# Kernel tuning notes

Measured on AMD Instinct MI355X. Metric: run time of the kernel, lower is better.

Reference implementation:

```python
import jax, jax.numpy as jnp
import numpy as np
from jax import lax

B, N, C = 4, 16384, 256
NH, HD = 8, 32          # num_heads, head_dim
SR = 4                  # spatial reduction ratio
LMAX = 6144             # max per-batch query length (static pad size)
QLENS = np.array([2048, 6144, 3072, 5120], dtype=np.int32)
TQ = int(QLENS.sum())   # 16384 total ragged queries
SCALE = HD ** -0.5


def setup_inputs() -> dict:
    key = jax.random.key(0)
    ks = jax.random.split(key, 6)
    w = lambda k, s: jax.random.normal(k, s, jnp.float32) * 0.02
    return {
        "x": jax.random.normal(ks[0], (B, N, C), jnp.float32),
        "q": jax.random.normal(ks[1], (TQ, C), jnp.float32),
        "H": 128,
        "W": 128,
        "q_lengths": jnp.asarray(QLENS),
        "w_q": w(ks[2], (C, C)),        # stored [in, out] (= torch W.T)
        "w_kv": w(ks[3], (C, 2 * C)),
        "sr_w": w(ks[4], (C, C, SR, SR)),  # OIHW
        "sr_b": jnp.zeros((C,), jnp.float32),
        "ln_g": jnp.ones((C,), jnp.float32),
        "ln_b": jnp.zeros((C,), jnp.float32),
        "proj_w": w(ks[5], (C, C)),
        "proj_b": jnp.zeros((C,), jnp.float32),
    }


def reference(x, q, H, W, q_lengths, w_q, w_kv, sr_w, sr_b, ln_g, ln_b, proj_w, proj_b):
    # q projection -> per-head ragged queries [NH, TQ, HD]
    qh = (q @ w_q).reshape(TQ, NH, HD).transpose(1, 0, 2)

    # spatial reduction of KV source: conv(k=SR, stride=SR) + LayerNorm
    x_ = x.transpose(0, 2, 1).reshape(B, C, H, W)
    x_ = lax.conv_general_dilated(x_, sr_w, (SR, SR), "VALID",
                                  dimension_numbers=("NCHW", "OIHW", "NCHW"))
    x_ = x_ + sr_b[None, :, None, None]
    x_ = x_.reshape(B, C, -1).transpose(0, 2, 1)  # [B, Nkv, C]
    mu = x_.mean(-1, keepdims=True)
    var = ((x_ - mu) ** 2).mean(-1, keepdims=True)
    x_ = (x_ - mu) * lax.rsqrt(var + 1e-5) * ln_g + ln_b

    # kv projection -> [NH, B, Nkv, HD] each
    kv = (x_ @ w_kv).reshape(B, -1, 2, NH, HD)
    k = kv[:, :, 0].transpose(2, 0, 1, 3)
    v = kv[:, :, 1].transpose(2, 0, 1, 3)

    # ragged -> padded layout for the variable-length attention
    batch_ids = jnp.repeat(jnp.arange(B), q_lengths, total_repeat_length=TQ)
    offsets = jnp.cumsum(q_lengths) - q_lengths
    pos = jnp.arange(TQ) - offsets[batch_ids]
    qp = jnp.zeros((NH, B, LMAX, HD), qh.dtype).at[:, batch_ids, pos].set(qh)

    # per-batch attention over reduced keys (padded rows are discarded below)
    attn = jax.nn.softmax(jnp.einsum("hbld,hbkd->hblk", qp, k) * SCALE, axis=-1)
    op = jnp.einsum("hblk,hbkd->hbld", attn, v)

    # gather valid ragged outputs back: [NH, TQ, HD] -> [TQ, C]
    o = op[:, batch_ids, pos].transpose(1, 0, 2).reshape(TQ, C)
    return o @ proj_w + proj_b
```

## Files before the change

### kernel.cpp

```cpp
#include <hip/hip_runtime.h>
#include <hip/hip_bf16.h>


using bf16 = __hip_bfloat16;
using f32x4 = __attribute__((ext_vector_type(4))) float;
using bf16x8 = __attribute__((ext_vector_type(8))) short;

#define DEVINL __device__ __forceinline__
#define AS1 __attribute__((address_space(1)))
#define AS3 __attribute__((address_space(3)))

DEVINL f32x4 mfma16(bf16x8 a, bf16x8 b, f32x4 c) {
    return __builtin_amdgcn_mfma_f32_16x16x32_bf16(a, b, c, 0, 0, 0);
}

DEVINL unsigned short f2bf(float f) {
    union { float f; unsigned u; } x; x.f = f;
    unsigned u = x.u;
    u += 0x7fffu + ((u >> 16) & 1u);
    return (unsigned short)(u >> 16);
}

DEVINL unsigned pk_rtz(float a, float b) {
    return __builtin_amdgcn_perm(__float_as_uint(b), __float_as_uint(a), 0x07060302u);
}

DEVINL float ex2(float x) { return __builtin_amdgcn_exp2f(x); }

DEVINL void gl16(const bf16* g, bf16* l) {
    __builtin_amdgcn_global_load_lds(
        (const AS1 void*)(unsigned long long)(uintptr_t)g,
        (AS3 void*)(unsigned)(uintptr_t)l, 16, 0, 0);
}
DEVINL void gl16f(const float* g, float* l) {
    __builtin_amdgcn_global_load_lds(
        (const AS1 void*)(unsigned long long)(uintptr_t)g,
        (AS3 void*)(unsigned)(uintptr_t)l, 16, 0, 0);
}

__global__ __launch_bounds__(256) void prep_kernel(
    const float* __restrict__ w_q, const float* __restrict__ w_kv,
    const float* __restrict__ proj_w, const float* __restrict__ sr_w,
    const float* __restrict__ q,
    bf16* __restrict__ wqT, bf16* __restrict__ wkvT, bf16* __restrict__ wprT,
    bf16* __restrict__ wcv, bf16* __restrict__ q_bf)
{
    const int bb = blockIdx.x;
    if (bb < 256) {
        int idx = bb * 256 + threadIdx.x;
        int k = idx & 255, n = idx >> 8;
        wqT[idx] = __float2bfloat16(w_q[k * 256 + n]);
    } else if (bb < 768) {
        int idx = (bb - 256) * 256 + threadIdx.x;
        int k = idx & 255, n = idx >> 8;
        wkvT[idx] = __float2bfloat16(w_kv[k * 512 + n]);
    } else if (bb < 1024) {
        int idx = (bb - 768) * 256 + threadIdx.x;
        int k = idx & 255, n = idx >> 8;
        wprT[idx] = __float2bfloat16(proj_w[k * 256 + n]);
    } else if (bb < 5120) {
        int idx = (bb - 1024) * 256 + threadIdx.x;
        int o = idx >> 12, rest = idx & 4095, dydx = rest >> 8, c = rest & 255;
        wcv[idx] = __float2bfloat16(sr_w[((o << 8) + c) * 16 + dydx]);
    } else {
        int i = (bb - 5120) * 256 + threadIdx.x;
        float4 a = ((const float4*)q)[i * 2];
        float4 b = ((const float4*)q)[i * 2 + 1];
        uint4 u;
        u.x = f2bf(a.x) | ((unsigned)f2bf(a.y) << 16);
        u.y = f2bf(a.z) | ((unsigned)f2bf(a.w) << 16);
        u.z = f2bf(b.x) | ((unsigned)f2bf(b.y) << 16);
        u.w = f2bf(b.z) | ((unsigned)f2bf(b.w) << 16);
        ((uint4*)q_bf)[i] = u;
    }
}

template<int EMODE>
__global__ __launch_bounds__(256, 4) void gemm_kernel(
    const bf16* __restrict__ A, const bf16* __restrict__ WT,
    const float* __restrict__ bias,
    bf16* __restrict__ outb, float* __restrict__ outf, bf16* __restrict__ out2,
    int M, int N, int K, int KS)
{
    __shared__ alignas(16) bf16 As[2][64 * 64];
    __shared__ alignas(16) bf16 Bs[2][64 * 64];
    const int cpx = gridDim.x >> 3;
    const int bx = (blockIdx.x & 7) * cpx + (blockIdx.x >> 3);
    const int ntn = N >> 6;
    const int tm = bx / ntn, tn = bx % ntn;
    const int tid = threadIdx.x, lane = tid & 63, wid = tid >> 6;
    const int l15 = lane & 15, g = lane >> 4;
    const int wm = (wid >> 1) << 5, wn = (wid & 1) << 5;
    f32x4 acc[2][2] = {};

    int r_[2], cs_[2];
#pragma unroll
    for (int j = 0; j < 2; ++j) {
        int idx = (wid * 2 + j) * 64 + lane;
        r_[j] = idx >> 3;
        cs_[j] = ((idx & 7) ^ (r_[j] & 7)) << 3;
    }
    const bf16* Arow = &A[(size_t)(tm * 64) * K];
    const bf16* Brow = &WT[(size_t)(tn * 64) * K];

    const int kbeg = blockIdx.y * KS;
    const int nsteps = KS >> 6;

    auto stage = [&](int buf, int k0) {
#pragma unroll
        for (int j = 0; j < 2; ++j) {
            gl16(Arow + (size_t)r_[j] * K + (k0 + cs_[j]), &As[buf][(wid * 2 + j) * 512]);
            gl16(Brow + (size_t)r_[j] * K + (k0 + cs_[j]), &Bs[buf][(wid * 2 + j) * 512]);
        }
    };

    stage(0, kbeg);
    __syncthreads();

    for (int t = 0; t < nsteps; ++t) {
        const int buf = t & 1;
        if (t + 1 < nsteps) stage(buf ^ 1, kbeg + (t + 1) * 64);
#pragma unroll
        for (int kk = 0; kk < 2; ++kk) {
            const int sw = l15 & 7;
            const int co = ((kk * 4 + g) ^ sw) << 3;
            bf16x8 a0 = *(const bf16x8*)&As[buf][(wm + l15) * 64 + co];
            bf16x8 a1 = *(const bf16x8*)&As[buf][(wm + 16 + l15) * 64 + co];
            bf16x8 b0 = *(const bf16x8*)&Bs[buf][(wn + l15) * 64 + co];
            bf16x8 b1 = *(const bf16x8*)&Bs[buf][(wn + 16 + l15) * 64 + co];
            acc[0][0] = mfma16(a0, b0, acc[0][0]);
            acc[0][1] = mfma16(a0, b1, acc[0][1]);
            acc[1][0] = mfma16(a1, b0, acc[1][0]);
            acc[1][1] = mfma16(a1, b1, acc[1][1]);
        }
        __syncthreads();
    }

    const float qscale = 0.1767766953f * 1.4426950409f;
#pragma unroll
    for (int mi = 0; mi < 2; ++mi)
#pragma unroll
    for (int ni = 0; ni < 2; ++ni)
#pragma unroll
    for (int r = 0; r < 4; ++r) {
        int row = tm * 64 + wm + mi * 16 + g * 4 + r;
        int col = tn * 64 + wn + ni * 16 + l15;
        float v = acc[mi][ni][r];
        if constexpr (EMODE == 0) {
            outb[(size_t)row * 256 + col] = __float2bfloat16(v * qscale);
        } else if constexpr (EMODE == 1) {
            outf[(size_t)row * 256 + col] = v + bias[col];
        } else if constexpr (EMODE == 2) {
            int bb = row >> 10, key = row & 1023;
            if (col < 256) {
                int hh = col >> 5, d = col & 31;
                outb[(size_t)(((bb << 3) + hh) * 1024 + key) * 32 + d] = __float2bfloat16(v);
            } else {
                int d = col - 256;
                int c = key & 31;
                int pos = (((c >> 2) & 3) << 3) + ((c >> 4) << 2) + (c & 3);
                int keyp = (key & ~31) | pos;
                out2[(size_t)(((bb << 3) + (d >> 5)) * 32 + (d & 31)) * 1024 + keyp] =
                    __float2bfloat16(v);
            }
        }
    }
}

__global__ __launch_bounds__(256, 6) void conv_gemm_kernel(
    const float* __restrict__ X, const bf16* __restrict__ WT,
    float* __restrict__ partials)
{
    __shared__ alignas(16) float Af[2][64 * 32];
    __shared__ alignas(16) bf16 Bs[2][64 * 32];
    const int K = 4096;
    const int swz = (blockIdx.x & 7) * 256 + (blockIdx.x >> 3);
    const int combo = swz >> 6;
    const int tm = swz & 63;
    const int tn = combo >> 3, slice = combo & 7;
    const int tid = threadIdx.x, lane = tid & 63, wid = tid >> 6;
    const int l15 = lane & 15, g = lane >> 4;
    const int wm = (wid >> 1) << 5, wn = (wid & 1) << 5;
    f32x4 acc[2][2] = {};

    size_t laneoffA[2];
#pragma unroll
    for (int j = 0; j < 2; ++j) {
        int call = wid * 2 + j;
        int rr = call * 8 + (lane >> 3);
        int pr = tm * 64 + rr;
        int b = pr >> 10, pi = pr & 1023;
        int ii = pi >> 5, jj = pi & 31;
        int c16 = lane & 7;
        int sc = (((c16 >> 1) ^ (rr & 3)) << 1) | (c16 & 1);
        laneoffA[j] = ((size_t)((b << 14) + (ii << 2) * 128 + (jj << 2))) * 256 + sc * 4;
    }
    const int rB = wid * 16 + (lane >> 2);
    const int scB = ((lane & 3) ^ (rB & 3)) << 3;
    const bf16* BrowP = &WT[(size_t)(tn * 64 + rB) * K + scB];

    const int kbeg = slice << 9;

    auto stage = [&](int buf, int t) {
        const int k0 = kbeg + t * 32;
        const int dydx = k0 >> 8;
        const int stepoff = ((dydx >> 2) * 128 + (dydx & 3)) * 256 + (k0 & 255);
#pragma unroll
        for (int j = 0; j < 2; ++j)
            gl16f(X + laneoffA[j] + stepoff, &Af[buf][(wid * 2 + j) * 256]);
        gl16(BrowP + k0, &Bs[buf][wid * 512]);
    };

    stage(0, 0);
    __syncthreads();

    for (int t = 0; t < 16; ++t) {
        const int buf = t & 1;
        if (t + 1 < 16) stage(buf ^ 1, t + 1);
        {
            const int sw = l15 & 3;
            const int ao = (g ^ sw) << 3;
            const float* ap0 = &Af[buf][(wm + l15) * 32 + ao];
            const float* ap1 = &Af[buf][(wm + 16 + l15) * 32 + ao];
            float4 lo0 = *(const float4*)ap0, hi0 = *(const float4*)(ap0 + 4);
            float4 lo1 = *(const float4*)ap1, hi1 = *(const float4*)(ap1 + 4);
            uint4 a0u, a1u;
            a0u.x = pk_rtz(lo0.x, lo0.y);  a0u.y = pk_rtz(lo0.z, lo0.w);
            a0u.z = pk_rtz(hi0.x, hi0.y);  a0u.w = pk_rtz(hi0.z, hi0.w);
            a1u.x = pk_rtz(lo1.x, lo1.y);  a1u.y = pk_rtz(lo1.z, lo1.w);
            a1u.z = pk_rtz(hi1.x, hi1.y);  a1u.w = pk_rtz(hi1.z, hi1.w);
            union { uint4 u; bf16x8 v; } a0c, a1c; a0c.u = a0u; a1c.u = a1u;
            bf16x8 b0 = *(const bf16x8*)&Bs[buf][(wn + l15) * 32 + ao];
            bf16x8 b1 = *(const bf16x8*)&Bs[buf][(wn + 16 + l15) * 32 + ao];
            acc[0][0] = mfma16(a0c.v, b0, acc[0][0]);
            acc[0][1] = mfma16(a0c.v, b1, acc[0][1]);
            acc[1][0] = mfma16(a1c.v, b0, acc[1][0]);
            acc[1][1] = mfma16(a1c.v, b1, acc[1][1]);
        }
        __syncthreads();
    }

#pragma unroll
    for (int mi = 0; mi < 2; ++mi)
#pragma unroll
    for (int ni = 0; ni < 2; ++ni)
#pragma unroll
    for (int r = 0; r < 4; ++r) {
        int row = tm * 64 + wm + mi * 16 + g * 4 + r;
        int col = tn * 64 + wn + ni * 16 + l15;
        partials[((size_t)slice * 4096 + row) * 256 + col] = acc[mi][ni][r];
    }
}

__global__ __launch_bounds__(256) void ln_kernel(const float* __restrict__ pp,
                                                 const float* __restrict__ cb,
                                                 const float* __restrict__ gw,
                                                 const float* __restrict__ bw,
                                                 bf16* __restrict__ out) {
    int row = blockIdx.x * 4 + (threadIdx.x >> 6);
    int lane = threadIdx.x & 63;
    const size_t base = (size_t)row * 256 + lane * 4;
    float4 v = *(const float4*)&pp[base];
#pragma unroll
    for (int s = 1; s < 8; ++s) {
        const float4 t = *(const float4*)&pp[(size_t)s * (4096 * 256) + base];
        v.x += t.x; v.y += t.y; v.z += t.z; v.w += t.w;
    }
    const float4 cbv = *(const float4*)&cb[lane * 4];
    v.x += cbv.x; v.y += cbv.y; v.z += cbv.z; v.w += cbv.w;

    float s = v.x + v.y + v.z + v.w;
#pragma unroll
    for (int m = 1; m < 64; m <<= 1) s += __shfl_xor(s, m, 64);
    float mu = s * 0.00390625f;
    float d0 = v.x - mu, d1 = v.y - mu, d2 = v.z - mu, d3 = v.w - mu;
    float qv = d0 * d0 + d1 * d1 + d2 * d2 + d3 * d3;
#pragma unroll
    for (int m = 1; m < 64; m <<= 1) qv += __shfl_xor(qv, m, 64);
    float rstd = rsqrtf(qv * 0.00390625f + 1e-5f);
    const float4 gg = *(const float4*)&gw[lane * 4];
    const float4 bb = *(const float4*)&bw[lane * 4];
    uint2 u;
    u.x = f2bf(d0 * rstd * gg.x + bb.x) | ((unsigned)f2bf(d1 * rstd * gg.y + bb.y) << 16);
    u.y = f2bf(d2 * rstd * gg.z + bb.z) | ((unsigned)f2bf(d3 * rstd * gg.w + bb.w) << 16);
    *(uint2*)&out[(size_t)row * 256 + lane * 4] = u;
}

__global__ __launch_bounds__(256, 4) void attn_kernel(
    const bf16* __restrict__ qh, const bf16* __restrict__ kh,
    const bf16* __restrict__ vt, bf16* __restrict__ obf)
{
    __shared__ alignas(16) bf16 Kl[2][128 * 32];
    __shared__ alignas(16) bf16 Vl[2][32 * 128];
    const int bid = blockIdx.x;
    const int h = bid & 7;
    const int tile = bid >> 3;
    const int row0 = tile << 7;
    const int b = (row0 < 2048) ? 0 : (row0 < 8192) ? 1 : (row0 < 11264) ? 2 : 3;
    const int tid = threadIdx.x, lane = tid & 63, w = tid >> 6;
    const int l15 = lane & 15, g = lane >> 4;
    const int qbase = row0 + (w << 5);
    const int bh = (b << 3) + h;

    bf16x8 qfA = *(const bf16x8*)&qh[(size_t)(qbase + l15) * 256 + h * 32 + g * 8];
    bf16x8 qfB = *(const bf16x8*)&qh[(size_t)(qbase + 16 + l15) * 256 + h * 32 + g * 8];

    bf16x8 ones;
    {
        unsigned ov = (l15 == 0) ? 0x3f803f80u : 0u;
        unsigned* op = (unsigned*)&ones;
        op[0] = ov; op[1] = ov; op[2] = ov; op[3] = ov;
    }

    f32x4 o0A = {0.f,0.f,0.f,0.f}, o1A = o0A, o2A = o0A;
    f32x4 o0B = o0A, o1B = o0A, o2B = o0A;
    const f32x4 z = {0.f, 0.f, 0.f, 0.f};

    const int skey = lane >> 2;
    const int skc  = (lane & 3) ^ (skey & 3);
    const int svd  = lane >> 4;
    const int svc  = lane & 15;
    const bf16* kbase = kh + (size_t)bh * 1024 * 32;
    const bf16* vbase = vt + (size_t)bh * 32 * 1024;

    auto stage = [&](int buf, int kb) {
        if (w < 2) {
#pragma unroll
            for (int jj = 0; jj < 4; ++jj) {
                int j = w * 4 + jj;
                int key = (j << 4) + skey;
                gl16(kbase + (size_t)(kb + key) * 32 + (skc << 3), &Kl[buf][j * 512]);
            }
        } else {
#pragma unroll
            for (int jj = 0; jj < 4; ++jj) {
                int j = (w - 2) * 4 + jj;
                int d = (j << 2) + svd;
                gl16(vbase + (size_t)d * 1024 + kb + ((svc ^ (d & 7)) << 3),
                     &Vl[buf][j * 512]);
            }
        }
    };

    stage(0, 0);
    __syncthreads();

    const int kc = g ^ (l15 & 3);
    const int vsw = l15 & 7;

    for (int t = 0; t < 8; ++t) {
        const int buf = t & 1;
        if (t < 7) stage(buf ^ 1, (t + 1) << 7);
#pragma unroll
        for (int s = 0; s < 4; ++s) {
            bf16x8 k0 = *(const bf16x8*)&Kl[buf][((s << 5) + l15) * 32 + (kc << 3)];
            bf16x8 k1 = *(const bf16x8*)&Kl[buf][((s << 5) + 16 + l15) * 32 + (kc << 3)];
            bf16x8 v0 = *(const bf16x8*)&Vl[buf][(l15 << 7) + ((((s << 2) + g) ^ vsw) << 3)];
            bf16x8 v1 = *(const bf16x8*)&Vl[buf][((16 + l15) << 7) + ((((s << 2) + g) ^ vsw) << 3)];

            f32x4 s0A = mfma16(k0, qfA, z);
            f32x4 s1A = mfma16(k1, qfA, z);
            f32x4 s0B = mfma16(k0, qfB, z);
            f32x4 s1B = mfma16(k1, qfB, z);

            uint4 pAu, pBu;
            pAu.x = pk_rtz(ex2(s0A[0]), ex2(s0A[1]));
            pAu.y = pk_rtz(ex2(s0A[2]), ex2(s0A[3]));
            pAu.z = pk_rtz(ex2(s1A[0]), ex2(s1A[1]));
            pAu.w = pk_rtz(ex2(s1A[2]), ex2(s1A[3]));
            pBu.x = pk_rtz(ex2(s0B[0]), ex2(s0B[1]));
            pBu.y = pk_rtz(ex2(s0B[2]), ex2(s0B[3]));
            pBu.z = pk_rtz(ex2(s1B[0]), ex2(s1B[1]));
            pBu.w = pk_rtz(ex2(s1B[2]), ex2(s1B[3]));
            union { uint4 u; bf16x8 v; } cA, cB;
            cA.u = pAu; cB.u = pBu;

            o0A = mfma16(cA.v, v0, o0A);
            o1A = mfma16(cA.v, v1, o1A);
            o2A = mfma16(cA.v, ones, o2A);
            o0B = mfma16(cB.v, v0, o0B);
            o1B = mfma16(cB.v, v1, o1B);
            o2B = mfma16(cB.v, ones, o2B);
        }
        __syncthreads();
    }

#pragma unroll
    for (int r = 0; r < 4; ++r) {
        float invA = 1.f / __shfl(o2A[r], g << 4, 64);
        float invB = 1.f / __shfl(o2B[r], g << 4, 64);
        size_t orowA = (size_t)(qbase + (g << 2) + r) * 256 + h * 32;
        size_t orowB = (size_t)(qbase + 16 + (g << 2) + r) * 256 + h * 32;
        obf[orowA + l15]      = __float2bfloat16(o0A[r] * invA);
        obf[orowA + 16 + l15] = __float2bfloat16(o1A[r] * invA);
        obf[orowB + l15]      = __float2bfloat16(o0B[r] * invB);
        obf[orowB + 16 + l15] = __float2bfloat16(o1B[r] * invB);
    }
}


extern "C" void kernel_launch(void* const* d_in, const int* in_sizes, int n_in,
                              void* d_out, int out_size, void* d_ws, size_t ws_size,
                              hipStream_t stream)
{
    const float* x      = (const float*)d_in[0];
    const float* q      = (const float*)d_in[1];
    const float* w_q    = (const float*)d_in[5];
    const float* w_kv   = (const float*)d_in[6];
    const float* sr_w   = (const float*)d_in[7];
    const float* sr_b   = (const float*)d_in[8];
    const float* ln_g   = (const float*)d_in[9];
    const float* ln_b   = (const float*)d_in[10];
    const float* proj_w = (const float*)d_in[11];
    const float* proj_b = (const float*)d_in[12];

    char* w = (char*)d_ws;
    bf16* q_bf = (bf16*)(w + 0);
    bf16* qh   = (bf16*)(w + 8388608);
    bf16* wqT  = (bf16*)(w + 16777216);
    bf16* wkvT = (bf16*)(w + 16908288);
    bf16* wprT = (bf16*)(w + 17170432);
    bf16* wcv  = (bf16*)(w + 17301504);
    bf16* xln  = (bf16*)(w + 19398656);
    bf16* kh   = (bf16*)(w + 21495808);
    bf16* vt   = (bf16*)(w + 23592960);
    bf16* obf  = (bf16*)(w + 25690112);
    float* partials = (float*)(w + 34078720);
    float* out = (float*)d_out;

    prep_kernel<<<7168, 256, 0, stream>>>(w_q, w_kv, proj_w, sr_w, q,
                                          wqT, wkvT, wprT, wcv, q_bf);
    gemm_kernel<0><<<1024, 256, 0, stream>>>(q_bf, wqT, nullptr, qh, nullptr, nullptr,
                                             16384, 256, 256, 256);
    conv_gemm_kernel<<<2048, 256, 0, stream>>>(x, wcv, partials);
    ln_kernel<<<1024, 256, 0, stream>>>(partials, sr_b, ln_g, ln_b, xln);
    gemm_kernel<2><<<512, 256, 0, stream>>>(xln, wkvT, nullptr, kh, nullptr, vt,
                                            4096, 512, 256, 256);
    attn_kernel<<<1024, 256, 0, stream>>>(qh, kh, vt, obf);
    gemm_kernel<1><<<1024, 256, 0, stream>>>(obf, wprT, proj_b, nullptr, out, nullptr,
                                             16384, 256, 256, 256);
}
```

Baseline: 112.7 us.

## Halve conv split-K slices, re-layout LDS tiles k-major, reuse output buffer for partials

The conv GEMM now uses 4 split-K slices of 1024 instead of 8 of 512, which doubles per-block loop length and halves the partial-sum traffic the LayerNorm kernel must reduce. The shared-memory A/B tiles change to a k-major layout with XOR row swizzling, and the block-to-tile mapping moves to a 2D grid with XCD-aware placement. Partials are written into the output buffer, which is only overwritten later by the final projection. In exchange the grid has half as many blocks, so the GPU may be less full.

```diff
diff --git a/kernel.cpp b/kernel.cpp
--- a/kernel.cpp
+++ b/kernel.cpp
@@ -171,67 +171,75 @@
     const float* __restrict__ X, const bf16* __restrict__ WT,
     float* __restrict__ partials)
 {
-    __shared__ alignas(16) float Af[2][64 * 32];
-    __shared__ alignas(16) bf16 Bs[2][64 * 32];
+    __shared__ alignas(16) float Af[2][512 * 4];
+    __shared__ alignas(16) bf16 Bs[2][256 * 8];
     const int K = 4096;
-    const int swz = (blockIdx.x & 7) * 256 + (blockIdx.x >> 3);
-    const int combo = swz >> 6;
-    const int tm = swz & 63;
-    const int tn = combo >> 3, slice = combo & 7;
+    const int bx = blockIdx.x;
+    const int xcd = bx & 7;
+    const int tn = (bx >> 3) & 3;
+    const int tm = xcd * 8 + (bx >> 5);
+    const int slice = blockIdx.y;
     const int tid = threadIdx.x, lane = tid & 63, wid = tid >> 6;
     const int l15 = lane & 15, g = lane >> 4;
     const int wm = (wid >> 1) << 5, wn = (wid & 1) << 5;
     f32x4 acc[2][2] = {};
 
     size_t laneoffA[2];
-#pragma unroll
-    for (int j = 0; j < 2; ++j) {
-        int call = wid * 2 + j;
-        int rr = call * 8 + (lane >> 3);
-        int pr = tm * 64 + rr;
+    int ldsA[2];
+#pragma unroll
+    for (int jj = 0; jj < 2; ++jj) {
+        int c = (wid * 2 + jj) * 64 + lane;
+        int k4 = c >> 6;
+        int row = (c & 63) ^ (k4 & 7);
+        int pr = tm * 64 + row;
         int b = pr >> 10, pi = pr & 1023;
-        int ii = pi >> 5, jj = pi & 31;
-        int c16 = lane & 7;
-        int sc = (((c16 >> 1) ^ (rr & 3)) << 1) | (c16 & 1);
-        laneoffA[j] = ((size_t)((b << 14) + (ii << 2) * 128 + (jj << 2))) * 256 + sc * 4;
-    }
-    const int rB = wid * 16 + (lane >> 2);
-    const int scB = ((lane & 3) ^ (rB & 3)) << 3;
-    const bf16* BrowP = &WT[(size_t)(tn * 64 + rB) * K + scB];
-
-    const int kbeg = slice << 9;
+        int ii = pi >> 5, jc = pi & 31;
+        laneoffA[jj] = ((size_t)((b << 14) + ii * 512 + jc * 4)) * 256 + k4 * 4;
+        ldsA[jj] = (wid * 2 + jj) * 256;
+    }
+    const bf16* laneBp;
+    int ldsB;
+    {
+        int c = wid * 64 + lane;
+        int k8 = c >> 6;
+        int n = (c & 63) ^ k8;
+        laneBp = &WT[(size_t)(tn * 64 + n) * K + k8 * 8];
+        ldsB = wid * 512;
+    }
+
+    const int kbeg = slice << 10;
 
     auto stage = [&](int buf, int t) {
         const int k0 = kbeg + t * 32;
         const int dydx = k0 >> 8;
         const int stepoff = ((dydx >> 2) * 128 + (dydx & 3)) * 256 + (k0 & 255);
 #pragma unroll
-        for (int j = 0; j < 2; ++j)
-            gl16f(X + laneoffA[j] + stepoff, &Af[buf][(wid * 2 + j) * 256]);
-        gl16(BrowP + k0, &Bs[buf][wid * 512]);
+        for (int jj = 0; jj < 2; ++jj)
+            gl16f(X + laneoffA[jj] + stepoff, &Af[buf][ldsA[jj]]);
+        gl16(laneBp + k0, &Bs[buf][ldsB]);
     };
 
     stage(0, 0);
     __syncthreads();
 
-    for (int t = 0; t < 16; ++t) {
+    for (int t = 0; t < 32; ++t) {
         const int buf = t & 1;
-        if (t + 1 < 16) stage(buf ^ 1, t + 1);
+        if (t + 1 < 32) stage(buf ^ 1, t + 1);
         {
-            const int sw = l15 & 3;
-            const int ao = (g ^ sw) << 3;
-            const float* ap0 = &Af[buf][(wm + l15) * 32 + ao];
-            const float* ap1 = &Af[buf][(wm + 16 + l15) * 32 + ao];
-            float4 lo0 = *(const float4*)ap0, hi0 = *(const float4*)(ap0 + 4);
-            float4 lo1 = *(const float4*)ap1, hi1 = *(const float4*)(ap1 + 4);
+            const int k4a = g << 1, k4b = k4a + 1;
+            const int r0 = wm + l15, r1 = wm + 16 + l15;
+            float4 lo0 = *(const float4*)&Af[buf][(k4a * 64 + (r0 ^ (k4a & 7))) * 4];
+            float4 hi0 = *(const float4*)&Af[buf][(k4b * 64 + (r0 ^ (k4b & 7))) * 4];
+            float4 lo1 = *(const float4*)&Af[buf][(k4a * 64 + (r1 ^ (k4a & 7))) * 4];
+            float4 hi1 = *(const float4*)&Af[buf][(k4b * 64 + (r1 ^ (k4b & 7))) * 4];
             uint4 a0u, a1u;
             a0u.x = pk_rtz(lo0.x, lo0.y);  a0u.y = pk_rtz(lo0.z, lo0.w);
             a0u.z = pk_rtz(hi0.x, hi0.y);  a0u.w = pk_rtz(hi0.z, hi0.w);
             a1u.x = pk_rtz(lo1.x, lo1.y);  a1u.y = pk_rtz(lo1.z, lo1.w);
             a1u.z = pk_rtz(hi1.x, hi1.y);  a1u.w = pk_rtz(hi1.z, hi1.w);
             union { uint4 u; bf16x8 v; } a0c, a1c; a0c.u = a0u; a1c.u = a1u;
-            bf16x8 b0 = *(const bf16x8*)&Bs[buf][(wn + l15) * 32 + ao];
-            bf16x8 b1 = *(const bf16x8*)&Bs[buf][(wn + 16 + l15) * 32 + ao];
+            bf16x8 b0 = *(const bf16x8*)&Bs[buf][(g * 64 + ((wn + l15) ^ g)) * 8];
+            bf16x8 b1 = *(const bf16x8*)&Bs[buf][(g * 64 + ((wn + 16 + l15) ^ g)) * 8];
             acc[0][0] = mfma16(a0c.v, b0, acc[0][0]);
             acc[0][1] = mfma16(a0c.v, b1, acc[0][1]);
             acc[1][0] = mfma16(a1c.v, b0, acc[1][0]);
@@ -262,7 +270,7 @@
     const size_t base = (size_t)row * 256 + lane * 4;
     float4 v = *(const float4*)&pp[base];
 #pragma unroll
-    for (int s = 1; s < 8; ++s) {
+    for (int s = 1; s < 4; ++s) {
         const float4 t = *(const float4*)&pp[(size_t)s * (4096 * 256) + base];
         v.x += t.x; v.y += t.y; v.z += t.z; v.w += t.w;
     }
@@ -425,14 +433,14 @@
     bf16* kh   = (bf16*)(w + 21495808);
     bf16* vt   = (bf16*)(w + 23592960);
     bf16* obf  = (bf16*)(w + 25690112);
-    float* partials = (float*)(w + 34078720);
+    float* partials = (float*)d_out;
     float* out = (float*)d_out;
 
     prep_kernel<<<7168, 256, 0, stream>>>(w_q, w_kv, proj_w, sr_w, q,
                                           wqT, wkvT, wprT, wcv, q_bf);
     gemm_kernel<0><<<1024, 256, 0, stream>>>(q_bf, wqT, nullptr, qh, nullptr, nullptr,
                                              16384, 256, 256, 256);
-    conv_gemm_kernel<<<2048, 256, 0, stream>>>(x, wcv, partials);
+    conv_gemm_kernel<<<dim3(256, 4), 256, 0, stream>>>(x, wcv, partials);
     ln_kernel<<<1024, 256, 0, stream>>>(partials, sr_b, ln_g, ln_b, xln);
     gemm_kernel<2><<<512, 256, 0, stream>>>(xln, wkvT, nullptr, kh, nullptr, vt,
                                             4096, 512, 256, 256);
```

Result: slower. 116.4 us (+3.3%).
